# Kernel tuning notes

Measured on AMD Instinct MI355X. Metric: run time of the kernel, lower is better.

Reference implementation:

```python
import jax, jax.numpy as jnp
import numpy as np
from jax import lax

SEQ = 32768
I = 128   # input_size
H = 512   # hidden_layer_size


def lstm_scan(xs, W_ih, W_hh, b_ih, b_hh):
    """Single-layer LSTM over time (PyTorch gate order i,f,g,o), batch=1.
    xs: [T, in], W_ih: [4h, in], W_hh: [4h, h], biases: [4h]. Returns [T, h]."""
    h_dim = W_hh.shape[1]
    x_gates = xs @ W_ih.T + (b_ih + b_hh)  # precompute input contribution [T, 4h]

    def step(carry, xg):
        h, c = carry
        gates = xg + h @ W_hh.T
        i, f, g, o = jnp.split(gates, 4)
        i = jax.nn.sigmoid(i)
        f = jax.nn.sigmoid(f)
        g = jnp.tanh(g)
        o = jax.nn.sigmoid(o)
        c = f * c + i * g
        h = o * jnp.tanh(c)
        return (h, c), h

    init = (jnp.zeros((h_dim,), xs.dtype), jnp.zeros((h_dim,), xs.dtype))
    _, hs = lax.scan(step, init, x_gates)
    return hs


def setup_inputs() -> dict:
    key = jax.random.key(0)
    ks = jax.random.split(key, 9)
    u = lambda k, shape, fan: jax.random.uniform(k, shape, jnp.float32, -1.0, 1.0) / np.sqrt(fan)
    return {
        "input_seq": jax.random.normal(ks[0], (SEQ, I), jnp.float32),
        # layer 1: input I -> hidden H
        "W_ih1": u(ks[1], (4 * H, I), H),
        "W_hh1": u(ks[2], (4 * H, H), H),
        "b_ih1": u(ks[3], (4 * H,), H),
        "b_hh1": u(ks[4], (4 * H,), H),
        # layer 2: hidden H -> input I
        "W_ih2": u(ks[5], (4 * I, H), I),
        "W_hh2": u(ks[6], (4 * I, I), I),
        "b_ih2": u(ks[7], (4 * I,), I),
        "b_hh2": u(ks[8], (4 * I,), I),
    }


def reference(input_seq, W_ih1, W_hh1, b_ih1, b_hh1, W_ih2, W_hh2, b_ih2, b_hh2):
    h1 = lstm_scan(input_seq, W_ih1, W_hh1, b_ih1, b_hh1)   # [T, H]
    h2 = lstm_scan(h1, W_ih2, W_hh2, b_ih2, b_hh2)          # [T, I]
    return h2.reshape(-1)                                    # predictions.view(-1)
```

## Files before the change

### kernel.cpp

```cpp
#include <hip/hip_runtime.h>
#include <math.h>


#define T_STEPS 32768
#define L1WG    16
#define NWG     24
#define BLK     512
#define RD      8

#define ABT_OFF  9
#define TAG_OFF  32
#define H1_OFF   1024
#define H2_OFF   (H1_OFF + RD * 512 * 2)
#define WS_WORDS (H2_OFF + RD * 128 * 2)

typedef unsigned int uint4v __attribute__((ext_vector_type(4)));

#define PIN(v) asm volatile("" : "+v"(v))

__device__ __forceinline__ float sigm(float x) { return 1.0f / (1.0f + __expf(-x)); }
__device__ __forceinline__ float tanh_fast(float x) { return 1.0f - 2.0f / (__expf(2.0f * x) + 1.0f); }

__device__ __forceinline__ unsigned ld_u32_sc1(const unsigned* p) {
    unsigned r;
    asm volatile("global_load_dword %0, %1, off sc1\n\ts_waitcnt vmcnt(0)"
                 : "=v"(r) : "v"(p) : "memory");
    return r;
}
__device__ __forceinline__ void st_u32_sc1(unsigned* p, unsigned v) {
    asm volatile("global_store_dword %0, %1, off sc1" :: "v"(p), "v"(v) : "memory");
}
__device__ __forceinline__ void st_u64_sc1(unsigned long long* p, unsigned long long v) {
    asm volatile("global_store_dwordx2 %0, %1, off sc1" :: "v"(p), "v"(v) : "memory");
}
__device__ __forceinline__ void ld2x16_sc1(const unsigned long long* p, uint4v& A, uint4v& B) {
    asm volatile("global_load_dwordx4 %0, %2, off sc1\n\t"
                 "global_load_dwordx4 %1, %3, off sc1\n\t"
                 "s_waitcnt vmcnt(0)"
                 : "=&v"(A), "=&v"(B) : "v"(p), "v"(p + 2) : "memory");
}
__device__ __forceinline__ void ld1x16_sc1(const unsigned long long* p, uint4v& A) {
    asm volatile("global_load_dwordx4 %0, %1, off sc1\n\ts_waitcnt vmcnt(0)"
                 : "=&v"(A) : "v"(p) : "memory");
}

__global__ void lstm_init(unsigned int* ws)
{
    int i = blockIdx.x * blockDim.x + threadIdx.x;
    if (i < WS_WORDS) ws[i] = 0u;
}

__global__ __launch_bounds__(BLK, 2) void lstm_persist(
    const float* __restrict__ x,
    const float* __restrict__ Wih1,
    const float* __restrict__ Whh1,
    const float* __restrict__ bih1,
    const float* __restrict__ bhh1,
    const float* __restrict__ Wih2,
    const float* __restrict__ Whh2,
    const float* __restrict__ bih2,
    const float* __restrict__ bhh2,
    float* __restrict__ out,
    unsigned int* ws)
{
    const int role = blockIdx.x;
    const int tid  = threadIdx.x;
    const int wave = tid >> 6;
    const int lane = tid & 63;

    __shared__ __align__(16) float h1buf[2][16 * 36];
    __shared__ __align__(16) float h2buf[2][8 * 20];
    __shared__ unsigned s_ab[1];

    unsigned* abf  = ws + ABT_OFF;
    unsigned* tags = ws + TAG_OFF;
    unsigned long long* h1r = (unsigned long long*)(ws + H1_OFF);
    unsigned long long* h2r = (unsigned long long*)(ws + H2_OFF);

    if (tid == 0) s_ab[0] = 0u;

    const bool isL1 = role < L1WG;

    if (isL1) {
        const int rt = tid >> 4;
        const int ct = tid & 15;
        const int hb = role * 32;

        float wA[4][32], wB[4][8], bia[4];
#pragma unroll
        for (int q = 0; q < 4; ++q) {
            const int grow = q * 512 + hb + rt;
            const float4* pa = (const float4*)(Whh1 + (size_t)grow * 512 + ct * 32);
#pragma unroll
            for (int c = 0; c < 8; ++c) {
                float4 f = pa[c];
                wA[q][c * 4 + 0] = f.x; wA[q][c * 4 + 1] = f.y;
                wA[q][c * 4 + 2] = f.z; wA[q][c * 4 + 3] = f.w;
            }
            const float4* pb = (const float4*)(Wih1 + (size_t)grow * 128 + ct * 8);
            float4 b0 = pb[0], b1 = pb[1];
            wB[q][0] = b0.x; wB[q][1] = b0.y; wB[q][2] = b0.z; wB[q][3] = b0.w;
            wB[q][4] = b1.x; wB[q][5] = b1.y; wB[q][6] = b1.z; wB[q][7] = b1.w;
            bia[q] = bih1[grow] + bhh1[grow];
        }
#pragma unroll
        for (int q = 0; q < 4; ++q) {
#pragma unroll
            for (int j = 0; j < 32; ++j) PIN(wA[q][j]);
#pragma unroll
            for (int j = 0; j < 8; ++j)  PIN(wB[q][j]);
            PIN(bia[q]);
        }

        float cst = 0.0f;
        float4 vx0 = *(const float4*)(x + ct * 8);
        float4 vx1 = *(const float4*)(x + ct * 8 + 4);
        __syncthreads();

        for (int n = 0; n < T_STEPS; ++n) {
            if (wave == 3 && n >= 8 && (n & 3) == 0 && lane < NWG) {
                const int thr = n - 3;
                unsigned sp = 0;
                for (;;) {
                    int ok = ((int)ld_u32_sc1(&tags[lane]) >= thr);
                    if (__all(ok)) break;
                    if ((++sp & 255u) == 0u) {
                        if (ld_u32_sc1(abf) != 0u) { s_ab[0] = 1u; break; }
                        if (sp >= (1u << 21)) { st_u32_sc1(abf, 1u); s_ab[0] = 1u; break; }
                    }
                }
            }
            if (wave < 2) {
                const size_t off = (size_t)((n - 1) & (RD - 1)) * 512 + wave * 256 + lane * 4;
                const unsigned long long* p = h1r + off;
                const unsigned e = (unsigned)n;
                const int g = wave * 256 + lane * 4;
                bool done = false;
                unsigned sp = 0;
                for (;;) {
                    if (!done) {
                        uint4v A, B;
                        ld2x16_sc1(p, A, B);
                        if ((A.y == e) & (A.w == e) & (B.y == e) & (B.w == e)) {
                            float4 vals = make_float4(
                                __uint_as_float(A.x), __uint_as_float(A.z),
                                __uint_as_float(B.x), __uint_as_float(B.z));
                            *(float4*)&h1buf[n & 1][(g >> 5) * 36 + (g & 31)] = vals;
                            done = true;
                        }
                    }
                    if (__all(done)) break;
                    if ((++sp & 255u) == 0u) {
                        if (ld_u32_sc1(abf) != 0u) { s_ab[0] = 1u; break; }
                        if (sp >= (1u << 21)) { st_u32_sc1(abf, 1u); s_ab[0] = 1u; break; }
                    }
                }
            }

            __syncthreads();
            if (s_ab[0]) break;
            if (tid == 0) st_u32_sc1(&tags[role], (unsigned)(n + 1));

            float acc0 = 0.f, acc1 = 0.f, acc2 = 0.f, acc3 = 0.f;
            const float* hv = &h1buf[n & 1][ct * 36];
#pragma unroll
            for (int c = 0; c < 8; ++c) {
                float4 h4 = *(const float4*)(hv + c * 4);
                acc0 = fmaf(wA[0][c*4+0], h4.x, acc0); acc0 = fmaf(wA[0][c*4+1], h4.y, acc0);
                acc0 = fmaf(wA[0][c*4+2], h4.z, acc0); acc0 = fmaf(wA[0][c*4+3], h4.w, acc0);
                acc1 = fmaf(wA[1][c*4+0], h4.x, acc1); acc1 = fmaf(wA[1][c*4+1], h4.y, acc1);
                acc1 = fmaf(wA[1][c*4+2], h4.z, acc1); acc1 = fmaf(wA[1][c*4+3], h4.w, acc1);
                acc2 = fmaf(wA[2][c*4+0], h4.x, acc2); acc2 = fmaf(wA[2][c*4+1], h4.y, acc2);
                acc2 = fmaf(wA[2][c*4+2], h4.z, acc2); acc2 = fmaf(wA[2][c*4+3], h4.w, acc2);
                acc3 = fmaf(wA[3][c*4+0], h4.x, acc3); acc3 = fmaf(wA[3][c*4+1], h4.y, acc3);
                acc3 = fmaf(wA[3][c*4+2], h4.z, acc3); acc3 = fmaf(wA[3][c*4+3], h4.w, acc3);
            }
            {
                float sx[8] = { vx0.x, vx0.y, vx0.z, vx0.w, vx1.x, vx1.y, vx1.z, vx1.w };
#pragma unroll
                for (int j = 0; j < 8; ++j) {
                    acc0 = fmaf(wB[0][j], sx[j], acc0);
                    acc1 = fmaf(wB[1][j], sx[j], acc1);
                    acc2 = fmaf(wB[2][j], sx[j], acc2);
                    acc3 = fmaf(wB[3][j], sx[j], acc3);
                }
            }
            {
                const int tn = (n + 1 < T_STEPS) ? (n + 1) : (T_STEPS - 1);
                vx0 = *(const float4*)(x + (size_t)tn * 128 + ct * 8);
                vx1 = *(const float4*)(x + (size_t)tn * 128 + ct * 8 + 4);
            }
#pragma unroll
            for (int m = 8; m >= 1; m >>= 1) {
                acc0 += __shfl_xor(acc0, m, 64);
                acc1 += __shfl_xor(acc1, m, 64);
                acc2 += __shfl_xor(acc2, m, 64);
                acc3 += __shfl_xor(acc3, m, 64);
            }
            const float ii = sigm(acc0 + bia[0]);
            const float ff = sigm(acc1 + bia[1]);
            const float g2 = tanh_fast(acc2 + bia[2]);
            const float oo = sigm(acc3 + bia[3]);
            cst = ff * cst + ii * g2;
            const float h = oo * tanh_fast(cst);

            if (ct == 0) {
                const unsigned long long pair =
                    ((unsigned long long)(unsigned)(n + 1) << 32) |
                    (unsigned long long)__float_as_uint(h);
                st_u64_sc1(&h1r[(size_t)(n & (RD - 1)) * 512 + hb + rt], pair);
            }
        }
    } else {
        const int rt  = tid >> 5;
        const int ct  = tid & 31;
        const int hb2 = (role - L1WG) * 16;

        float wA[4][16], wB[4][4], bia[4];
#pragma unroll
        for (int q = 0; q < 4; ++q) {
            const int grow = q * 128 + hb2 + rt;
            const float4* pa = (const float4*)(Wih2 + (size_t)grow * 512 + ct * 16);
#pragma unroll
            for (int c = 0; c < 4; ++c) {
                float4 f = pa[c];
                wA[q][c * 4 + 0] = f.x; wA[q][c * 4 + 1] = f.y;
                wA[q][c * 4 + 2] = f.z; wA[q][c * 4 + 3] = f.w;
            }
            float4 b0 = *(const float4*)(Whh2 + (size_t)grow * 128 + ct * 4);
            wB[q][0] = b0.x; wB[q][1] = b0.y; wB[q][2] = b0.z; wB[q][3] = b0.w;
            bia[q] = bih2[grow] + bhh2[grow];
        }
#pragma unroll
        for (int q = 0; q < 4; ++q) {
#pragma unroll
            for (int j = 0; j < 16; ++j) PIN(wA[q][j]);
#pragma unroll
            for (int j = 0; j < 4; ++j)  PIN(wB[q][j]);
            PIN(bia[q]);
        }

        float cst = 0.0f;
        __syncthreads();

        for (int n = 1; n <= T_STEPS; ++n) {
            const int tau = n - 1;
            if (wave == 3 && n >= 8 && (n & 3) == 0 && lane < NWG) {
                const int thr = n - 3;
                unsigned sp = 0;
                for (;;) {
                    int ok = ((int)ld_u32_sc1(&tags[lane]) >= thr);
                    if (__all(ok)) break;
                    if ((++sp & 255u) == 0u) {
                        if (ld_u32_sc1(abf) != 0u) { s_ab[0] = 1u; break; }
                        if (sp >= (1u << 21)) { st_u32_sc1(abf, 1u); s_ab[0] = 1u; break; }
                    }
                }
            }
            if (wave < 2) {
                const size_t off = (size_t)(tau & (RD - 1)) * 512 + wave * 256 + lane * 4;
                const unsigned long long* p = h1r + off;
                const unsigned e = (unsigned)n;
                const int g = wave * 256 + lane * 4;
                bool done = false;
                unsigned sp = 0;
                for (;;) {
                    if (!done) {
                        uint4v A, B;
                        ld2x16_sc1(p, A, B);
                        if ((A.y == e) & (A.w == e) & (B.y == e) & (B.w == e)) {
                            float4 vals = make_float4(
                                __uint_as_float(A.x), __uint_as_float(A.z),
                                __uint_as_float(B.x), __uint_as_float(B.z));
                            *(float4*)&h1buf[n & 1][(g >> 5) * 36 + (g & 31)] = vals;
                            done = true;
                        }
                    }
                    if (__all(done)) break;
                    if ((++sp & 255u) == 0u) {
                        if (ld_u32_sc1(abf) != 0u) { s_ab[0] = 1u; break; }
                        if (sp >= (1u << 21)) { st_u32_sc1(abf, 1u); s_ab[0] = 1u; break; }
                    }
                }
            }
            if (wave == 2) {
                const size_t off = (size_t)((tau - 1) & (RD - 1)) * 128 + lane * 2;
                const unsigned long long* p = h2r + off;
                const unsigned e = (unsigned)tau;
                const int pi = lane * 2;
                bool done = false;
                unsigned sp = 0;
                for (;;) {
                    if (!done) {
                        uint4v A;
                        ld1x16_sc1(p, A);
                        if ((A.y == e) & (A.w == e)) {
                            float2 v2 = make_float2(__uint_as_float(A.x),
                                                    __uint_as_float(A.z));
                            *(float2*)&h2buf[n & 1][(pi >> 4) * 20 + (pi & 15)] = v2;
                            done = true;
                        }
                    }
                    if (__all(done)) break;
                    if ((++sp & 255u) == 0u) {
                        if (ld_u32_sc1(abf) != 0u) { s_ab[0] = 1u; break; }
                        if (sp >= (1u << 21)) { st_u32_sc1(abf, 1u); s_ab[0] = 1u; break; }
                    }
                }
            }

            __syncthreads();
            if (s_ab[0]) break;
            if (tid == 0) st_u32_sc1(&tags[role], (unsigned)(n + 1));

            float acc0 = 0.f, acc1 = 0.f, acc2 = 0.f, acc3 = 0.f;
            const float* hv = &h1buf[n & 1][(ct >> 1) * 36 + (ct & 1) * 16];
#pragma unroll
            for (int c = 0; c < 4; ++c) {
                float4 h4 = *(const float4*)(hv + c * 4);
                acc0 = fmaf(wA[0][c*4+0], h4.x, acc0); acc0 = fmaf(wA[0][c*4+1], h4.y, acc0);
                acc0 = fmaf(wA[0][c*4+2], h4.z, acc0); acc0 = fmaf(wA[0][c*4+3], h4.w, acc0);
                acc1 = fmaf(wA[1][c*4+0], h4.x, acc1); acc1 = fmaf(wA[1][c*4+1], h4.y, acc1);
                acc1 = fmaf(wA[1][c*4+2], h4.z, acc1); acc1 = fmaf(wA[1][c*4+3], h4.w, acc1);
                acc2 = fmaf(wA[2][c*4+0], h4.x, acc2); acc2 = fmaf(wA[2][c*4+1], h4.y, acc2);
                acc2 = fmaf(wA[2][c*4+2], h4.z, acc2); acc2 = fmaf(wA[2][c*4+3], h4.w, acc2);
                acc3 = fmaf(wA[3][c*4+0], h4.x, acc3); acc3 = fmaf(wA[3][c*4+1], h4.y, acc3);
                acc3 = fmaf(wA[3][c*4+2], h4.z, acc3); acc3 = fmaf(wA[3][c*4+3], h4.w, acc3);
            }
            {
                float4 s4 = *(const float4*)&h2buf[n & 1][(ct >> 2) * 20 + (ct & 3) * 4];
                float sv[4] = { s4.x, s4.y, s4.z, s4.w };
#pragma unroll
                for (int j = 0; j < 4; ++j) {
                    acc0 = fmaf(wB[0][j], sv[j], acc0);
                    acc1 = fmaf(wB[1][j], sv[j], acc1);
                    acc2 = fmaf(wB[2][j], sv[j], acc2);
                    acc3 = fmaf(wB[3][j], sv[j], acc3);
                }
            }
#pragma unroll
            for (int m = 16; m >= 1; m >>= 1) {
                acc0 += __shfl_xor(acc0, m, 64);
                acc1 += __shfl_xor(acc1, m, 64);
                acc2 += __shfl_xor(acc2, m, 64);
                acc3 += __shfl_xor(acc3, m, 64);
            }
            const float ii = sigm(acc0 + bia[0]);
            const float ff = sigm(acc1 + bia[1]);
            const float g2 = tanh_fast(acc2 + bia[2]);
            const float oo = sigm(acc3 + bia[3]);
            cst = ff * cst + ii * g2;
            const float h = oo * tanh_fast(cst);

            if (ct == 0) {
                const unsigned long long pair =
                    ((unsigned long long)(unsigned)n << 32) |
                    (unsigned long long)__float_as_uint(h);
                st_u64_sc1(&h2r[(size_t)(tau & (RD - 1)) * 128 + hb2 + rt], pair);
                out[(size_t)tau * 128 + hb2 + rt] = h;
            }
        }
    }
}

extern "C" void kernel_launch(void* const* d_in, const int* in_sizes, int n_in,
                              void* d_out, int out_size, void* d_ws, size_t ws_size,
                              hipStream_t stream)
{
    const float* x    = (const float*)d_in[0];
    const float* Wih1 = (const float*)d_in[1];
    const float* Whh1 = (const float*)d_in[2];
    const float* bih1 = (const float*)d_in[3];
    const float* bhh1 = (const float*)d_in[4];
    const float* Wih2 = (const float*)d_in[5];
    const float* Whh2 = (const float*)d_in[6];
    const float* bih2 = (const float*)d_in[7];
    const float* bhh2 = (const float*)d_in[8];
    unsigned int* ws  = (unsigned int*)d_ws;

    hipLaunchKernelGGL(lstm_init, dim3(44), dim3(256), 0, stream, ws);
    hipLaunchKernelGGL(lstm_persist, dim3(NWG), dim3(BLK), 0, stream,
                       x, Wih1, Whh1, bih1, bhh1, Wih2, Whh2, bih2, bhh2,
                       (float*)d_out, ws);
}
```

Measured before the change: 90.95 ms.

## Poll hidden state directly in every thread, dropping LDS staging and a barrier

Each thread now polls the tagged global h-ring for exactly the 16 hidden values it needs, using eight 16-byte loads, and folds them into its FMAs right away. This removes the shared-memory staging buffers, the wave-specialised pollers and the barrier that used to sit between receiving h and computing on it. Layer 1 is remapped to 32 columns by 16 rows with two hidden units per thread, and the h stores now happen before the block barrier. The cost is that every thread issues global polling loads, which raises memory traffic and register pressure. The PIN register-pinning asm is removed and the timeout and abort-check intervals are shortened.

Result: slower. 132.0 ms (+45.1%).

```diff
diff --git a/kernel.cpp b/kernel.cpp
--- a/kernel.cpp
+++ b/kernel.cpp
@@ -16,8 +16,6 @@
 
 typedef unsigned int uint4v __attribute__((ext_vector_type(4)));
 
-#define PIN(v) asm volatile("" : "+v"(v))
-
 __device__ __forceinline__ float sigm(float x) { return 1.0f / (1.0f + __expf(-x)); }
 __device__ __forceinline__ float tanh_fast(float x) { return 1.0f - 2.0f / (__expf(2.0f * x) + 1.0f); }
 
@@ -39,9 +37,25 @@
                  "s_waitcnt vmcnt(0)"
                  : "=&v"(A), "=&v"(B) : "v"(p), "v"(p + 2) : "memory");
 }
-__device__ __forceinline__ void ld1x16_sc1(const unsigned long long* p, uint4v& A) {
-    asm volatile("global_load_dwordx4 %0, %1, off sc1\n\ts_waitcnt vmcnt(0)"
-                 : "=&v"(A) : "v"(p) : "memory");
+__device__ __forceinline__ void ld8x16_sc1(const unsigned long long* p,
+    uint4v& A0, uint4v& A1, uint4v& A2, uint4v& A3,
+    uint4v& A4, uint4v& A5, uint4v& A6, uint4v& A7)
+{
+    asm volatile(
+        "global_load_dwordx4 %0, %8, off sc1\n\t"
+        "global_load_dwordx4 %1, %9, off sc1\n\t"
+        "global_load_dwordx4 %2, %10, off sc1\n\t"
+        "global_load_dwordx4 %3, %11, off sc1\n\t"
+        "global_load_dwordx4 %4, %12, off sc1\n\t"
+        "global_load_dwordx4 %5, %13, off sc1\n\t"
+        "global_load_dwordx4 %6, %14, off sc1\n\t"
+        "global_load_dwordx4 %7, %15, off sc1\n\t"
+        "s_waitcnt vmcnt(0)"
+        : "=&v"(A0), "=&v"(A1), "=&v"(A2), "=&v"(A3),
+          "=&v"(A4), "=&v"(A5), "=&v"(A6), "=&v"(A7)
+        : "v"(p), "v"(p + 2), "v"(p + 4), "v"(p + 6),
+          "v"(p + 8), "v"(p + 10), "v"(p + 12), "v"(p + 14)
+        : "memory");
 }
 
 __global__ void lstm_init(unsigned int* ws)
@@ -67,9 +81,9 @@
     const int tid  = threadIdx.x;
     const int wave = tid >> 6;
     const int lane = tid & 63;
-
-    __shared__ __align__(16) float h1buf[2][16 * 36];
-    __shared__ __align__(16) float h2buf[2][8 * 20];
+    const int ct   = tid & 31;
+    const int rt   = tid >> 5;
+
     __shared__ unsigned s_ab[1];
 
     unsigned* abf  = ws + ABT_OFF;
@@ -82,39 +96,30 @@
     const bool isL1 = role < L1WG;
 
     if (isL1) {
-        const int rt = tid >> 4;
-        const int ct = tid & 15;
         const int hb = role * 32;
 
-        float wA[4][32], wB[4][8], bia[4];
-#pragma unroll
-        for (int q = 0; q < 4; ++q) {
-            const int grow = q * 512 + hb + rt;
-            const float4* pa = (const float4*)(Whh1 + (size_t)grow * 512 + ct * 32);
-#pragma unroll
-            for (int c = 0; c < 8; ++c) {
-                float4 f = pa[c];
-                wA[q][c * 4 + 0] = f.x; wA[q][c * 4 + 1] = f.y;
-                wA[q][c * 4 + 2] = f.z; wA[q][c * 4 + 3] = f.w;
-            }
-            const float4* pb = (const float4*)(Wih1 + (size_t)grow * 128 + ct * 8);
-            float4 b0 = pb[0], b1 = pb[1];
-            wB[q][0] = b0.x; wB[q][1] = b0.y; wB[q][2] = b0.z; wB[q][3] = b0.w;
-            wB[q][4] = b1.x; wB[q][5] = b1.y; wB[q][6] = b1.z; wB[q][7] = b1.w;
-            bia[q] = bih1[grow] + bhh1[grow];
+        float wA[2][4][16], wB[2][4][4], bia[2][4];
+#pragma unroll
+        for (int hh = 0; hh < 2; ++hh) {
+#pragma unroll
+            for (int q = 0; q < 4; ++q) {
+                const int grow = q * 512 + hb + hh * 16 + rt;
+                const float4* pa = (const float4*)(Whh1 + (size_t)grow * 512 + ct * 16);
+#pragma unroll
+                for (int c = 0; c < 4; ++c) {
+                    float4 f = pa[c];
+                    wA[hh][q][c * 4 + 0] = f.x; wA[hh][q][c * 4 + 1] = f.y;
+                    wA[hh][q][c * 4 + 2] = f.z; wA[hh][q][c * 4 + 3] = f.w;
+                }
+                float4 fb = *(const float4*)(Wih1 + (size_t)grow * 128 + ct * 4);
+                wB[hh][q][0] = fb.x; wB[hh][q][1] = fb.y;
+                wB[hh][q][2] = fb.z; wB[hh][q][3] = fb.w;
+                bia[hh][q] = bih1[grow] + bhh1[grow];
+            }
         }
-#pragma unroll
-        for (int q = 0; q < 4; ++q) {
-#pragma unroll
-            for (int j = 0; j < 32; ++j) PIN(wA[q][j]);
-#pragma unroll
-            for (int j = 0; j < 8; ++j)  PIN(wB[q][j]);
-            PIN(bia[q]);
-        }
-
-        float cst = 0.0f;
-        float4 vx0 = *(const float4*)(x + ct * 8);
-        float4 vx1 = *(const float4*)(x + ct * 8 + 4);
+
+        float cst0 = 0.0f, cst1 = 0.0f;
+        float4 vx = *(const float4*)(x + ct * 4);
         __syncthreads();
 
         for (int n = 0; n < T_STEPS; ++n) {
@@ -126,94 +131,106 @@
                     if (__all(ok)) break;
                     if ((++sp & 255u) == 0u) {
                         if (ld_u32_sc1(abf) != 0u) { s_ab[0] = 1u; break; }
-                        if (sp >= (1u << 21)) { st_u32_sc1(abf, 1u); s_ab[0] = 1u; break; }
-                    }
-                }
-            }
-            if (wave < 2) {
-                const size_t off = (size_t)((n - 1) & (RD - 1)) * 512 + wave * 256 + lane * 4;
-                const unsigned long long* p = h1r + off;
+                        if (sp >= (1u << 20)) { st_u32_sc1(abf, 1u); s_ab[0] = 1u; break; }
+                    }
+                }
+            }
+
+            float a00 = 0.f, a01 = 0.f, a02 = 0.f, a03 = 0.f;
+            float a10 = 0.f, a11 = 0.f, a12 = 0.f, a13 = 0.f;
+            {
                 const unsigned e = (unsigned)n;
-                const int g = wave * 256 + lane * 4;
+                const unsigned long long* p =
+                    h1r + (size_t)((n - 1) & (RD - 1)) * 512 + ct * 16;
                 bool done = false;
                 unsigned sp = 0;
                 for (;;) {
                     if (!done) {
-                        uint4v A, B;
-                        ld2x16_sc1(p, A, B);
-                        if ((A.y == e) & (A.w == e) & (B.y == e) & (B.w == e)) {
-                            float4 vals = make_float4(
-                                __uint_as_float(A.x), __uint_as_float(A.z),
-                                __uint_as_float(B.x), __uint_as_float(B.z));
-                            *(float4*)&h1buf[n & 1][(g >> 5) * 36 + (g & 31)] = vals;
+                        uint4v A0, A1, A2, A3, A4, A5, A6, A7;
+                        ld8x16_sc1(p, A0, A1, A2, A3, A4, A5, A6, A7);
+                        int ok = (A0.y == e) & (A0.w == e) & (A1.y == e) & (A1.w == e)
+                               & (A2.y == e) & (A2.w == e) & (A3.y == e) & (A3.w == e)
+                               & (A4.y == e) & (A4.w == e) & (A5.y == e) & (A5.w == e)
+                               & (A6.y == e) & (A6.w == e) & (A7.y == e) & (A7.w == e);
+                        if (ok) {
+                            uint4v W[8] = { A0, A1, A2, A3, A4, A5, A6, A7 };
+#pragma unroll
+                            for (int k = 0; k < 8; ++k) {
+                                const float v0 = __uint_as_float(W[k].x);
+                                const float v1 = __uint_as_float(W[k].z);
+                                a00 = fmaf(wA[0][0][2*k], v0, fmaf(wA[0][0][2*k+1], v1, a00));
+                                a01 = fmaf(wA[0][1][2*k], v0, fmaf(wA[0][1][2*k+1], v1, a01));
+                                a02 = fmaf(wA[0][2][2*k], v0, fmaf(wA[0][2][2*k+1], v1, a02));
+                                a03 = fmaf(wA[0][3][2*k], v0, fmaf(wA[0][3][2*k+1], v1, a03));
+                                a10 = fmaf(wA[1][0][2*k], v0, fmaf(wA[1][0][2*k+1], v1, a10));
+                                a11 = fmaf(wA[1][1][2*k], v0, fmaf(wA[1][1][2*k+1], v1, a11));
+                                a12 = fmaf(wA[1][2][2*k], v0, fmaf(wA[1][2][2*k+1], v1, a12));
+                                a13 = fmaf(wA[1][3][2*k], v0, fmaf(wA[1][3][2*k+1], v1, a13));
+                            }
+                            const float sx[4] = { vx.x, vx.y, vx.z, vx.w };
+#pragma unroll
+                            for (int j = 0; j < 4; ++j) {
+                                a00 = fmaf(wB[0][0][j], sx[j], a00);
+                                a01 = fmaf(wB[0][1][j], sx[j], a01);
+                                a02 = fmaf(wB[0][2][j], sx[j], a02);
+                                a03 = fmaf(wB[0][3][j], sx[j], a03);
+                                a10 = fmaf(wB[1][0][j], sx[j], a10);
+                                a11 = fmaf(wB[1][1][j], sx[j], a11);
+                                a12 = fmaf(wB[1][2][j], sx[j], a12);
+                                a13 = fmaf(wB[1][3][j], sx[j], a13);
+                            }
                             done = true;
                         }
                     }
                     if (__all(done)) break;
-                    if ((++sp & 255u) == 0u) {
-                        if (ld_u32_sc1(abf) != 0u) { s_ab[0] = 1u; break; }
-                        if (sp >= (1u << 21)) { st_u32_sc1(abf, 1u); s_ab[0] = 1u; break; }
-                    }
+                    if ((++sp & 63u) == 0u) {
+                        if (ld_u32_sc1(abf) != 0u) { s_ab[0] = 1u; break; }
+                        if (sp >= (1u << 20)) { st_u32_sc1(abf, 1u); s_ab[0] = 1u; break; }
+                    }
+                }
+            }
+
+            {
+                const int tn = (n + 1 < T_STEPS) ? (n + 1) : (T_STEPS - 1);
+                vx = *(const float4*)(x + (size_t)tn * 128 + ct * 4);
+            }
+
+#pragma unroll
+            for (int m = 16; m >= 1; m >>= 1) {
+                a00 += __shfl_xor(a00, m, 64); a01 += __shfl_xor(a01, m, 64);
+                a02 += __shfl_xor(a02, m, 64); a03 += __shfl_xor(a03, m, 64);
+                a10 += __shfl_xor(a10, m, 64); a11 += __shfl_xor(a11, m, 64);
+                a12 += __shfl_xor(a12, m, 64); a13 += __shfl_xor(a13, m, 64);
+            }
+
+            {
+                const float i0 = sigm(a00 + bia[0][0]);
+                const float f0 = sigm(a01 + bia[0][1]);
+                const float g0 = tanh_fast(a02 + bia[0][2]);
+                const float o0 = sigm(a03 + bia[0][3]);
+                cst0 = f0 * cst0 + i0 * g0;
+                const float h0 = o0 * tanh_fast(cst0);
+
+                const float i1 = sigm(a10 + bia[1][0]);
+                const float f1 = sigm(a11 + bia[1][1]);
+                const float g1 = tanh_fast(a12 + bia[1][2]);
+                const float o1 = sigm(a13 + bia[1][3]);
+                cst1 = f1 * cst1 + i1 * g1;
+                const float h1v = o1 * tanh_fast(cst1);
+
+                if (ct == 0) {
+                    const unsigned long long t64 = (unsigned long long)(unsigned)(n + 1) << 32;
+                    const size_t slot = (size_t)(n & (RD - 1)) * 512;
+                    st_u64_sc1(&h1r[slot + hb + rt],      t64 | (unsigned long long)__float_as_uint(h0));
+                    st_u64_sc1(&h1r[slot + hb + 16 + rt], t64 | (unsigned long long)__float_as_uint(h1v));
                 }
             }
 
             __syncthreads();
             if (s_ab[0]) break;
             if (tid == 0) st_u32_sc1(&tags[role], (unsigned)(n + 1));
-
-            float acc0 = 0.f, acc1 = 0.f, acc2 = 0.f, acc3 = 0.f;
-            const float* hv = &h1buf[n & 1][ct * 36];
-#pragma unroll
-            for (int c = 0; c < 8; ++c) {
-                float4 h4 = *(const float4*)(hv + c * 4);
-                acc0 = fmaf(wA[0][c*4+0], h4.x, acc0); acc0 = fmaf(wA[0][c*4+1], h4.y, acc0);
-                acc0 = fmaf(wA[0][c*4+2], h4.z, acc0); acc0 = fmaf(wA[0][c*4+3], h4.w, acc0);
-                acc1 = fmaf(wA[1][c*4+0], h4.x, acc1); acc1 = fmaf(wA[1][c*4+1], h4.y, acc1);
-                acc1 = fmaf(wA[1][c*4+2], h4.z, acc1); acc1 = fmaf(wA[1][c*4+3], h4.w, acc1);
-                acc2 = fmaf(wA[2][c*4+0], h4.x, acc2); acc2 = fmaf(wA[2][c*4+1], h4.y, acc2);
-                acc2 = fmaf(wA[2][c*4+2], h4.z, acc2); acc2 = fmaf(wA[2][c*4+3], h4.w, acc2);
-                acc3 = fmaf(wA[3][c*4+0], h4.x, acc3); acc3 = fmaf(wA[3][c*4+1], h4.y, acc3);
-                acc3 = fmaf(wA[3][c*4+2], h4.z, acc3); acc3 = fmaf(wA[3][c*4+3], h4.w, acc3);
-            }
-            {
-                float sx[8] = { vx0.x, vx0.y, vx0.z, vx0.w, vx1.x, vx1.y, vx1.z, vx1.w };
-#pragma unroll
-                for (int j = 0; j < 8; ++j) {
-                    acc0 = fmaf(wB[0][j], sx[j], acc0);
-                    acc1 = fmaf(wB[1][j], sx[j], acc1);
-                    acc2 = fmaf(wB[2][j], sx[j], acc2);
-                    acc3 = fmaf(wB[3][j], sx[j], acc3);
-                }
-            }
-            {
-                const int tn = (n + 1 < T_STEPS) ? (n + 1) : (T_STEPS - 1);
-                vx0 = *(const float4*)(x + (size_t)tn * 128 + ct * 8);
-                vx1 = *(const float4*)(x + (size_t)tn * 128 + ct * 8 + 4);
-            }
-#pragma unroll
-            for (int m = 8; m >= 1; m >>= 1) {
-                acc0 += __shfl_xor(acc0, m, 64);
-                acc1 += __shfl_xor(acc1, m, 64);
-                acc2 += __shfl_xor(acc2, m, 64);
-                acc3 += __shfl_xor(acc3, m, 64);
-            }
-            const float ii = sigm(acc0 + bia[0]);
-            const float ff = sigm(acc1 + bia[1]);
-            const float g2 = tanh_fast(acc2 + bia[2]);
-            const float oo = sigm(acc3 + bia[3]);
-            cst = ff * cst + ii * g2;
-            const float h = oo * tanh_fast(cst);
-
-            if (ct == 0) {
-                const unsigned long long pair =
-                    ((unsigned long long)(unsigned)(n + 1) << 32) |
-                    (unsigned long long)__float_as_uint(h);
-                st_u64_sc1(&h1r[(size_t)(n & (RD - 1)) * 512 + hb + rt], pair);
-            }
         }
     } else {
-        const int rt  = tid >> 5;
-        const int ct  = tid & 31;
         const int hb2 = (role - L1WG) * 16;
 
         float wA[4][16], wB[4][4], bia[4];
@@ -231,14 +248,6 @@
             wB[q][0] = b0.x; wB[q][1] = b0.y; wB[q][2] = b0.z; wB[q][3] = b0.w;
             bia[q] = bih2[grow] + bhh2[grow];
         }
-#pragma unroll
-        for (int q = 0; q < 4; ++q) {
-#pragma unroll
-            for (int j = 0; j < 16; ++j) PIN(wA[q][j]);
-#pragma unroll
-            for (int j = 0; j < 4; ++j)  PIN(wB[q][j]);
-            PIN(bia[q]);
-        }
 
         float cst = 0.0f;
         __syncthreads();
@@ -253,112 +262,105 @@
                     if (__all(ok)) break;
                     if ((++sp & 255u) == 0u) {
                         if (ld_u32_sc1(abf) != 0u) { s_ab[0] = 1u; break; }
-                        if (sp >= (1u << 21)) { st_u32_sc1(abf, 1u); s_ab[0] = 1u; break; }
-                    }
-                }
-            }
-            if (wave < 2) {
-                const size_t off = (size_t)(tau & (RD - 1)) * 512 + wave * 256 + lane * 4;
-                const unsigned long long* p = h1r + off;
+                        if (sp >= (1u << 20)) { st_u32_sc1(abf, 1u); s_ab[0] = 1u; break; }
+                    }
+                }
+            }
+
+            float a0 = 0.f, a1 = 0.f, a2 = 0.f, a3 = 0.f;
+
+            {
+                const unsigned e2 = (unsigned)tau;
+                const unsigned long long* p2 =
+                    h2r + (size_t)((tau - 1) & (RD - 1)) * 128 + ct * 4;
+                bool dn = false;
+                unsigned sp = 0;
+                for (;;) {
+                    if (!dn) {
+                        uint4v A, B;
+                        ld2x16_sc1(p2, A, B);
+                        if ((A.y == e2) & (A.w == e2) & (B.y == e2) & (B.w == e2)) {
+                            const float s0 = __uint_as_float(A.x);
+                            const float s1 = __uint_as_float(A.z);
+                            const float s2 = __uint_as_float(B.x);
+                            const float s3 = __uint_as_float(B.z);
+                            a0 = fmaf(wB[0][0], s0, fmaf(wB[0][1], s1, fmaf(wB[0][2], s2, fmaf(wB[0][3], s3, a0))));
+                            a1 = fmaf(wB[1][0], s0, fmaf(wB[1][1], s1, fmaf(wB[1][2], s2, fmaf(wB[1][3], s3, a1))));
+                            a2 = fmaf(wB[2][0], s0, fmaf(wB[2][1], s1, fmaf(wB[2][2], s2, fmaf(wB[2][3], s3, a2))));
+                            a3 = fmaf(wB[3][0], s0, fmaf(wB[3][1], s1, fmaf(wB[3][2], s2, fmaf(wB[3][3], s3, a3))));
+                            dn = true;
+                        }
+                    }
+                    if (__all(dn)) break;
+                    if ((++sp & 63u) == 0u) {
+                        if (ld_u32_sc1(abf) != 0u) { s_ab[0] = 1u; break; }
+                        if (sp >= (1u << 20)) { st_u32_sc1(abf, 1u); s_ab[0] = 1u; break; }
+                    }
+                }
+            }
+
+            {
                 const unsigned e = (unsigned)n;
-                const int g = wave * 256 + lane * 4;
+                const unsigned long long* p =
+                    h1r + (size_t)(tau & (RD - 1)) * 512 + ct * 16;
                 bool done = false;
                 unsigned sp = 0;
                 for (;;) {
                     if (!done) {
-                        uint4v A, B;
-                        ld2x16_sc1(p, A, B);
-                        if ((A.y == e) & (A.w == e) & (B.y == e) & (B.w == e)) {
-                            float4 vals = make_float4(
-                                __uint_as_float(A.x), __uint_as_float(A.z),
-                                __uint_as_float(B.x), __uint_as_float(B.z));
-                            *(float4*)&h1buf[n & 1][(g >> 5) * 36 + (g & 31)] = vals;
+                        uint4v A0, A1, A2, A3, A4, A5, A6, A7;
+                        ld8x16_sc1(p, A0, A1, A2, A3, A4, A5, A6, A7);
+                        int ok = (A0.y == e) & (A0.w == e) & (A1.y == e) & (A1.w == e)
+                               & (A2.y == e) & (A2.w == e) & (A3.y == e) & (A3.w == e)
+                               & (A4.y == e) & (A4.w == e) & (A5.y == e) & (A5.w == e)
+                               & (A6.y == e) & (A6.w == e) & (A7.y == e) & (A7.w == e);
+                        if (ok) {
+                            uint4v W[8] = { A0, A1, A2, A3, A4, A5, A6, A7 };
+#pragma unroll
+                            for (int k = 0; k < 8; ++k) {
+                                const float v0 = __uint_as_float(W[k].x);
+                                const float v1 = __uint_as_float(W[k].z);
+                                a0 = fmaf(wA[0][2*k], v0, fmaf(wA[0][2*k+1], v1, a0));
+                                a1 = fmaf(wA[1][2*k], v0, fmaf(wA[1][2*k+1], v1, a1));
+                                a2 = fmaf(wA[2][2*k], v0, fmaf(wA[2][2*k+1], v1, a2));
+                                a3 = fmaf(wA[3][2*k], v0, fmaf(wA[3][2*k+1], v1, a3));
+                            }
                             done = true;
                         }
                     }
                     if (__all(done)) break;
-                    if ((++sp & 255u) == 0u) {
-                        if (ld_u32_sc1(abf) != 0u) { s_ab[0] = 1u; break; }
-                        if (sp >= (1u << 21)) { st_u32_sc1(abf, 1u); s_ab[0] = 1u; break; }
-                    }
-                }
-            }
-            if (wave == 2) {
-                const size_t off = (size_t)((tau - 1) & (RD - 1)) * 128 + lane * 2;
-                const unsigned long long* p = h2r + off;
-                const unsigned e = (unsigned)tau;
-                const int pi = lane * 2;
-                bool done = false;
-                unsigned sp = 0;
-                for (;;) {
-                    if (!done) {
-                        uint4v A;
-                        ld1x16_sc1(p, A);
-                        if ((A.y == e) & (A.w == e)) {
-                            float2 v2 = make_float2(__uint_as_float(A.x),
-                                                    __uint_as_float(A.z));
-                            *(float2*)&h2buf[n & 1][(pi >> 4) * 20 + (pi & 15)] = v2;
-                            done = true;
-                        }
-                    }
-                    if (__all(done)) break;
-                    if ((++sp & 255u) == 0u) {
-                        if (ld_u32_sc1(abf) != 0u) { s_ab[0] = 1u; break; }
-                        if (sp >= (1u << 21)) { st_u32_sc1(abf, 1u); s_ab[0] = 1u; break; }
-                    }
+                    if ((++sp & 63u) == 0u) {
+                        if (ld_u32_sc1(abf) != 0u) { s_ab[0] = 1u; break; }
+                        if (sp >= (1u << 20)) { st_u32_sc1(abf, 1u); s_ab[0] = 1u; break; }
+                    }
+                }
+            }
+
+#pragma unroll
+            for (int m = 16; m >= 1; m >>= 1) {
+                a0 += __shfl_xor(a0, m, 64); a1 += __shfl_xor(a1, m, 64);
+                a2 += __shfl_xor(a2, m, 64); a3 += __shfl_xor(a3, m, 64);
+            }
+
+            {
+                const float ii = sigm(a0 + bia[0]);
+                const float ff = sigm(a1 + bia[1]);
+                const float gg = tanh_fast(a2 + bia[2]);
+                const float oo = sigm(a3 + bia[3]);
+                cst = ff * cst + ii * gg;
+                const float h = oo * tanh_fast(cst);
+
+                if (ct == 0) {
+                    const unsigned long long pair =
+                        ((unsigned long long)(unsigned)n << 32) |
+                        (unsigned long long)__float_as_uint(h);
+                    st_u64_sc1(&h2r[(size_t)(tau & (RD - 1)) * 128 + hb2 + rt], pair);
+                    out[(size_t)tau * 128 + hb2 + rt] = h;
                 }
             }
 
             __syncthreads();
             if (s_ab[0]) break;
             if (tid == 0) st_u32_sc1(&tags[role], (unsigned)(n + 1));
-
-            float acc0 = 0.f, acc1 = 0.f, acc2 = 0.f, acc3 = 0.f;
-            const float* hv = &h1buf[n & 1][(ct >> 1) * 36 + (ct & 1) * 16];
-#pragma unroll
-            for (int c = 0; c < 4; ++c) {
-                float4 h4 = *(const float4*)(hv + c * 4);
-                acc0 = fmaf(wA[0][c*4+0], h4.x, acc0); acc0 = fmaf(wA[0][c*4+1], h4.y, acc0);
-                acc0 = fmaf(wA[0][c*4+2], h4.z, acc0); acc0 = fmaf(wA[0][c*4+3], h4.w, acc0);
-                acc1 = fmaf(wA[1][c*4+0], h4.x, acc1); acc1 = fmaf(wA[1][c*4+1], h4.y, acc1);
-                acc1 = fmaf(wA[1][c*4+2], h4.z, acc1); acc1 = fmaf(wA[1][c*4+3], h4.w, acc1);
-                acc2 = fmaf(wA[2][c*4+0], h4.x, acc2); acc2 = fmaf(wA[2][c*4+1], h4.y, acc2);
-                acc2 = fmaf(wA[2][c*4+2], h4.z, acc2); acc2 = fmaf(wA[2][c*4+3], h4.w, acc2);
-                acc3 = fmaf(wA[3][c*4+0], h4.x, acc3); acc3 = fmaf(wA[3][c*4+1], h4.y, acc3);
-                acc3 = fmaf(wA[3][c*4+2], h4.z, acc3); acc3 = fmaf(wA[3][c*4+3], h4.w, acc3);
-            }
-            {
-                float4 s4 = *(const float4*)&h2buf[n & 1][(ct >> 2) * 20 + (ct & 3) * 4];
-                float sv[4] = { s4.x, s4.y, s4.z, s4.w };
-#pragma unroll
-                for (int j = 0; j < 4; ++j) {
-                    acc0 = fmaf(wB[0][j], sv[j], acc0);
-                    acc1 = fmaf(wB[1][j], sv[j], acc1);
-                    acc2 = fmaf(wB[2][j], sv[j], acc2);
-                    acc3 = fmaf(wB[3][j], sv[j], acc3);
-                }
-            }
-#pragma unroll
-            for (int m = 16; m >= 1; m >>= 1) {
-                acc0 += __shfl_xor(acc0, m, 64);
-                acc1 += __shfl_xor(acc1, m, 64);
-                acc2 += __shfl_xor(acc2, m, 64);
-                acc3 += __shfl_xor(acc3, m, 64);
-            }
-            const float ii = sigm(acc0 + bia[0]);
-            const float ff = sigm(acc1 + bia[1]);
-            const float g2 = tanh_fast(acc2 + bia[2]);
-            const float oo = sigm(acc3 + bia[3]);
-            cst = ff * cst + ii * g2;
-            const float h = oo * tanh_fast(cst);
-
-            if (ct == 0) {
-                const unsigned long long pair =
-                    ((unsigned long long)(unsigned)n << 32) |
-                    (unsigned long long)__float_as_uint(h);
-                st_u64_sc1(&h2r[(size_t)(tau & (RD - 1)) * 128 + hb2 + rt], pair);
-                out[(size_t)tau * 128 + hb2 + rt] = h;
-            }
         }
     }
 }
```
